# Optimization experiments

Measured on AMD Instinct MI355X. Metric: run time of the kernel, lower is better.

The kernel has to match this reference:

```python
import jax, jax.numpy as jnp
import numpy as np

B, C, H, W = 2, 256, 32, 32
D_MODEL = C
D_INNER = 2 * D_MODEL          # 512
D_STATE = 16
DT_RANK = (D_MODEL + 15) // 16  # 16
D_CONV = 4
LN_EPS = 1e-5


def setup_inputs() -> dict:
    key = jax.random.key(0)
    ks = jax.random.split(key, 32)

    def nrm(k, shape, s=0.02):
        return (jax.random.normal(k, shape) * s).astype(jnp.float32)

    inp = {"x": jax.random.normal(ks[0], (B, C, H, W), dtype=jnp.float32)}
    # LayerNorm params
    inp["ln1_w"] = jnp.ones((D_MODEL,), jnp.float32)
    inp["ln1_b"] = jnp.zeros((D_MODEL,), jnp.float32)
    inp["ln2_w"] = jnp.ones((D_MODEL,), jnp.float32)
    inp["ln2_b"] = jnp.zeros((D_MODEL,), jnp.float32)
    # Two MambaBlocks with identical structure
    for i, p in enumerate(["m1", "m2"]):
        o = 1 + i * 11
        inp[p + "_in_w"] = nrm(ks[o + 0], (D_MODEL, 2 * D_INNER))
        inp[p + "_in_b"] = jnp.zeros((2 * D_INNER,), jnp.float32)
        inp[p + "_conv_w"] = nrm(ks[o + 1], (D_INNER, 1, D_CONV), 0.1)
        inp[p + "_conv_b"] = jnp.zeros((D_INNER,), jnp.float32)
        inp[p + "_xproj_w"] = nrm(ks[o + 2], (D_INNER, DT_RANK + 2 * D_STATE))
        inp[p + "_dt_w"] = nrm(ks[o + 3], (DT_RANK, D_INNER), 0.1)
        inp[p + "_dt_b"] = (jax.random.uniform(ks[o + 4], (D_INNER,)) * 0.1 - 4.0).astype(jnp.float32)
        # S4D-real init: A[d, n] = n+1
        inp[p + "_A_log"] = jnp.log(jnp.broadcast_to(jnp.arange(1, D_STATE + 1, dtype=jnp.float32), (D_INNER, D_STATE)))
        inp[p + "_D"] = jnp.ones((D_INNER,), jnp.float32)
        inp[p + "_out_w"] = nrm(ks[o + 5], (D_INNER, D_MODEL))
        inp[p + "_out_b"] = jnp.zeros((D_MODEL,), jnp.float32)
    return inp


def layernorm(x, w, b):
    mu = jnp.mean(x, axis=-1, keepdims=True)
    var = jnp.mean(jnp.square(x - mu), axis=-1, keepdims=True)
    return (x - mu) * jax.lax.rsqrt(var + LN_EPS) * w + b


def mamba_block(x, in_w, in_b, conv_w, conv_b, xproj_w, dt_w, dt_b, A_log, Dp, out_w, out_b):
    # x: (b, h, w, c) -> flatten spatial dims into the scan sequence
    b, h, w, c = x.shape
    L = h * w
    u = x.reshape(b, L, c)
    xr = u @ in_w + in_b                       # (b, L, 2*d_inner)
    xs, res = jnp.split(xr, 2, axis=-1)
    # depthwise causal conv1d over L
    xc = jnp.transpose(xs, (0, 2, 1))          # (b, d_inner, L)
    xc = jax.lax.conv_general_dilated(
        xc, conv_w, (1,), [(D_CONV - 1, 0)],
        dimension_numbers=("NCH", "OIH", "NCH"),
        feature_group_count=D_INNER) + conv_b[None, :, None]
    xs = jax.nn.silu(jnp.transpose(xc, (0, 2, 1)))  # (b, L, d_inner)
    # input-dependent SSM params
    x_dbl = xs @ xproj_w                       # (b, L, dt_rank + 2*n)
    dt, Bm, Cm = jnp.split(x_dbl, [DT_RANK, DT_RANK + D_STATE], axis=-1)
    delta = jax.nn.softplus(dt @ dt_w + dt_b)  # (b, L, d_inner)
    A = -jnp.exp(A_log)                        # (d_inner, n)
    dA = jnp.exp(delta[..., None] * A)                         # (b, L, d, n)
    dBu = delta[..., None] * Bm[:, :, None, :] * xs[..., None]  # (b, L, d, n)

    def step(hst, ins):
        dA_t, dBu_t, C_t = ins
        hst = dA_t * hst + dBu_t               # (b, d, n)
        y_t = jnp.einsum("bdn,bn->bd", hst, C_t)
        return hst, y_t

    h0 = jnp.zeros((b, D_INNER, D_STATE), dtype=xs.dtype)
    _, ys = jax.lax.scan(step, h0,
                         (jnp.swapaxes(dA, 0, 1), jnp.swapaxes(dBu, 0, 1), jnp.swapaxes(Cm, 0, 1)))
    y = jnp.swapaxes(ys, 0, 1) + xs * Dp       # (b, L, d_inner)
    y = y * jax.nn.silu(res)
    out = y @ out_w + out_b                    # (b, L, c)
    return out.reshape(b, h, w, c)


def reference(x, ln1_w, ln1_b, ln2_w, ln2_b,
              m1_in_w, m1_in_b, m1_conv_w, m1_conv_b, m1_xproj_w, m1_dt_w, m1_dt_b, m1_A_log, m1_D, m1_out_w, m1_out_b,
              m2_in_w, m2_in_b, m2_conv_w, m2_conv_b, m2_xproj_w, m2_dt_w, m2_dt_b, m2_A_log, m2_D, m2_out_w, m2_out_b):
    xt = jnp.transpose(x, (0, 2, 3, 1))  # b c h w -> b h w c
    xt = xt + layernorm(mamba_block(xt, m1_in_w, m1_in_b, m1_conv_w, m1_conv_b, m1_xproj_w,
                                    m1_dt_w, m1_dt_b, m1_A_log, m1_D, m1_out_w, m1_out_b), ln1_w, ln1_b)
    xt = jnp.flip(xt, axis=3)  # flip channel axis, as in the original
    xt = xt + layernorm(mamba_block(xt, m2_in_w, m2_in_b, m2_conv_w, m2_conv_b, m2_xproj_w,
                                    m2_dt_w, m2_dt_b, m2_A_log, m2_D, m2_out_w, m2_out_b), ln2_w, ln2_b)
    xt = jnp.flip(xt, axis=3)
    return jnp.transpose(xt, (0, 3, 1, 2))  # b h w c -> b c h w
```

## Files before the change

kernel.cpp:

```cpp
#include <hip/hip_runtime.h>
#include <hip/hip_bf16.h>
#include <math.h>

#define L 1024
#define NB 2
#define DM 256
#define DI 512
#define DS 16
#define DR 16
#define NC 64
#define CL 16

typedef unsigned int u32;
typedef short s16x8 __attribute__((ext_vector_type(8)));
typedef float f32x4 __attribute__((ext_vector_type(4)));

__device__ __forceinline__ float sigmoidf_(float x){ return 1.f/(1.f+__expf(-x)); }

__device__ __forceinline__ unsigned short f2bf(float v){
  u32 x = __float_as_uint(v);
  u32 r = (x + 0x7fffu + ((x >> 16) & 1u)) >> 16;
  return (unsigned short)r;
}

__device__ __forceinline__ void gload_lds16(const void* g, void* l){
  __builtin_amdgcn_global_load_lds((const __attribute__((address_space(1))) u32*)g,
                                   (__attribute__((address_space(3))) u32*)l, 16, 0, 0);
}

__device__ __forceinline__ void wave_reduce2(float& a, float& b){
  #pragma unroll
  for (int m=32; m; m>>=1){ a += __shfl_xor(a, m, 64); b += __shfl_xor(b, m, 64); }
}

#define SEG1 262144
#define SEG2 294912
#define SEG3 131072
#define SEGP (SEG1+SEG2+SEG3)
__global__ __launch_bounds__(256) void k_prep(
    const float* __restrict__ inw1, const float* __restrict__ xpw1, const float* __restrict__ dtw1, const float* __restrict__ outw1,
    const float* __restrict__ inw2, const float* __restrict__ xpw2, const float* __restrict__ dtw2, const float* __restrict__ outw2,
    unsigned short* __restrict__ Wt1i, unsigned short* __restrict__ Wt1x, unsigned short* __restrict__ Wt1o,
    unsigned short* __restrict__ Wt2i, unsigned short* __restrict__ Wt2x, unsigned short* __restrict__ Wt2o){
  int g = blockIdx.x*256 + threadIdx.x;
  int p = g >= SEGP;
  int r = g - p*SEGP;
  const float* inw = p ? inw2 : inw1;  const float* xpw = p ? xpw2 : xpw1;
  const float* dtw = p ? dtw2 : dtw1;  const float* outw = p ? outw2 : outw1;
  unsigned short* Wti = p ? Wt2i : Wt1i; unsigned short* Wtx = p ? Wt2x : Wt1x;
  unsigned short* Wto = p ? Wt2o : Wt1o;
  if (r < SEG1){
    int n = r >> 8, k = r & 255;
    Wti[r] = f2bf(inw[(size_t)k*1024 + n]);
  } else if (r < SEG1+SEG2){
    int q = r - SEG1; int n = q >> 9, k = q & 511;
    float v;
    if (n < 512){
      float acc = 0.f;
      #pragma unroll
      for (int j=0;j<16;++j) acc = fmaf(xpw[k*48 + j], dtw[j*512 + n], acc);
      v = acc;
    } else if (n < 544){
      v = xpw[k*48 + 16 + (n - 512)];
    } else v = 0.f;
    Wtx[q] = f2bf(v);
  } else {
    int q = r - SEG1 - SEG2; int n = q >> 9, k = q & 511;
    Wto[q] = f2bf(outw[(size_t)k*256 + n]);
  }
}

__global__ __launch_bounds__(256) void k_transpose_in(const float* __restrict__ x,
    float* __restrict__ u, unsigned short* __restrict__ ub){
  __shared__ float T[64][65];
  int t = threadIdx.x;
  int bidx = blockIdx.x;
  int lt = bidx & 15, ct = (bidx >> 4) & 3, b = bidx >> 6;
  int l0 = lt*64, c0 = ct*64;
  int lsub = (t & 15)*4, csub = t >> 4;
  #pragma unroll
  for (int i=0;i<4;++i){
    int c = csub + i*16;
    float4 v = *(const float4*)(x + ((size_t)(b*256 + c0 + c))*1024 + l0 + lsub);
    T[lsub+0][c]=v.x; T[lsub+1][c]=v.y; T[lsub+2][c]=v.z; T[lsub+3][c]=v.w;
  }
  __syncthreads();
  int cw = (t & 15)*4, lw = t >> 4;
  #pragma unroll
  for (int i=0;i<4;++i){
    int l = lw + i*16;
    float4 v = make_float4(T[l][cw], T[l][cw+1], T[l][cw+2], T[l][cw+3]);
    size_t o = ((size_t)(b*1024 + l0 + l))*256 + c0 + cw;
    *(float4*)(u + o) = v;
    *(ushort4*)(ub + o) = make_ushort4(f2bf(v.x), f2bf(v.y), f2bf(v.z), f2bf(v.w));
  }
}

__global__ __launch_bounds__(256) void k_gemm_mfma(const unsigned short* __restrict__ A,
    const unsigned short* __restrict__ Wt, const float* __restrict__ bias,
    float* __restrict__ C, int M, int N, int K){
  __shared__ __align__(16) unsigned short As[64*64];
  __shared__ __align__(16) unsigned short Bs[64*64];
  int tid = threadIdx.x;
  int lane = tid & 63;
  int wid  = tid >> 6;
  int bm = blockIdx.y * 64, bn = blockIdx.x * 64;
  int wm = (wid >> 1) * 32, wn = (wid & 1) * 32;
  int lrow = lane & 15, lg = lane >> 4;
  int srow = tid >> 3;
  int ssl  = tid & 7;
  int sswz = ssl ^ (srow & 7);

  f32x4 acc[2][2] = {};

  for (int k0 = 0; k0 < K; k0 += 64){
    #pragma unroll
    for (int i = 0; i < 2; ++i){
      int row = srow + i*32;
      gload_lds16(A  + (size_t)(bm + row)*K + k0 + sswz*8, &As[row*64 + ssl*8]);
      gload_lds16(Wt + (size_t)(bn + row)*K + k0 + sswz*8, &Bs[row*64 + ssl*8]);
    }
    __syncthreads();
    #pragma unroll
    for (int ks = 0; ks < 2; ++ks){
      int kg = ks*4 + lg;
      int swz = (kg ^ (lrow & 7)) << 3;
      s16x8 a[2], b[2];
      #pragma unroll
      for (int f = 0; f < 2; ++f){
        a[f] = *(const s16x8*)&As[(wm + f*16 + lrow)*64 + swz];
        b[f] = *(const s16x8*)&Bs[(wn + f*16 + lrow)*64 + swz];
      }
      #pragma unroll
      for (int i = 0; i < 2; ++i)
        #pragma unroll
        for (int j = 0; j < 2; ++j)
          acc[i][j] = __builtin_amdgcn_mfma_f32_16x16x32_bf16(a[i], b[j], acc[i][j], 0, 0, 0);
    }
    __syncthreads();
  }
  #pragma unroll
  for (int j = 0; j < 2; ++j){
    int col = bn + wn + j*16 + lrow;
    if (col < N){
      float bv = bias ? bias[col] : 0.f;
      #pragma unroll
      for (int i = 0; i < 2; ++i){
        #pragma unroll
        for (int r = 0; r < 4; ++r){
          int row = bm + wm + i*16 + lg*4 + r;
          C[(size_t)row*N + col] = acc[i][j][r] + bv;
        }
      }
    }
  }
}

__global__ __launch_bounds__(256) void k_gemm_xproj(const unsigned short* __restrict__ A,
    const unsigned short* __restrict__ Wt, const float* __restrict__ dtb,
    float* __restrict__ dlt, float* __restrict__ BC, int M){
  const int K = 512;
  __shared__ __align__(16) unsigned short As[64*64];
  __shared__ __align__(16) unsigned short Bs[64*64];
  int tid = threadIdx.x;
  int lane = tid & 63;
  int wid  = tid >> 6;
  int bm = blockIdx.y * 64, bn = blockIdx.x * 64;
  int wm = (wid >> 1) * 32, wn = (wid & 1) * 32;
  int lrow = lane & 15, lg = lane >> 4;
  int srow = tid >> 3;
  int ssl  = tid & 7;
  int sswz = ssl ^ (srow & 7);

  f32x4 acc[2][2] = {};

  for (int k0 = 0; k0 < K; k0 += 64){
    #pragma unroll
    for (int i = 0; i < 2; ++i){
      int row = srow + i*32;
      gload_lds16(A  + (size_t)(bm + row)*K + k0 + sswz*8, &As[row*64 + ssl*8]);
      gload_lds16(Wt + (size_t)(bn + row)*K + k0 + sswz*8, &Bs[row*64 + ssl*8]);
    }
    __syncthreads();
    #pragma unroll
    for (int ks = 0; ks < 2; ++ks){
      int kg = ks*4 + lg;
      int swz = (kg ^ (lrow & 7)) << 3;
      s16x8 a[2], b[2];
      #pragma unroll
      for (int f = 0; f < 2; ++f){
        a[f] = *(const s16x8*)&As[(wm + f*16 + lrow)*64 + swz];
        b[f] = *(const s16x8*)&Bs[(wn + f*16 + lrow)*64 + swz];
      }
      #pragma unroll
      for (int i = 0; i < 2; ++i)
        #pragma unroll
        for (int j = 0; j < 2; ++j)
          acc[i][j] = __builtin_amdgcn_mfma_f32_16x16x32_bf16(a[i], b[j], acc[i][j], 0, 0, 0);
    }
    __syncthreads();
  }
  #pragma unroll
  for (int j = 0; j < 2; ++j){
    int col = bn + wn + j*16 + lrow;
    if (col < 512){
      float bv = dtb[col];
      #pragma unroll
      for (int i = 0; i < 2; ++i){
        #pragma unroll
        for (int r = 0; r < 4; ++r){
          int row = bm + wm + i*16 + lg*4 + r;
          float a = acc[i][j][r] + bv;
          dlt[(size_t)row*512 + col] = fmaxf(a, 0.f) + log1pf(__expf(-fabsf(a)));
        }
      }
    } else if (col < 544){
      #pragma unroll
      for (int i = 0; i < 2; ++i){
        #pragma unroll
        for (int r = 0; r < 4; ++r){
          int row = bm + wm + i*16 + lg*4 + r;
          BC[(size_t)row*32 + (col - 512)] = acc[i][j][r];
        }
      }
    }
  }
}

__global__ __launch_bounds__(256) void k_conv_silu(const float* __restrict__ xr, const float* __restrict__ cw,
    const float* __restrict__ cb, float* __restrict__ xsc, unsigned short* __restrict__ xscb){
  int g = blockIdx.x*256 + threadIdx.x;
  int d = g & 511; int l = (g >> 9) & 1023; int b = g >> 19;
  float acc = cb[d];
  const float* w = cw + d*4;
  #pragma unroll
  for (int k=0;k<4;++k){
    int j = l + k - 3;
    if (j >= 0) acc = fmaf(w[k], xr[((size_t)(b*L + j))*(2*DI) + d], acc);
  }
  float v = acc * sigmoidf_(acc);
  xsc[g] = v; xscb[g] = f2bf(v);
}

__global__ __launch_bounds__(256) void k_scan_partial(const float* __restrict__ delta, const float* __restrict__ xsc,
    const float* __restrict__ BC, const float* __restrict__ A_log,
    float* __restrict__ hend, float* __restrict__ Ssum){
  int g = blockIdx.x*256 + threadIdx.x;
  int d = g & 511; int bc = g >> 9;
  int c = bc & (NC-1); int b = bc >> 6;
  float A[DS];
  #pragma unroll
  for (int n=0;n<DS;++n) A[n] = -__expf(A_log[d*DS + n]);
  float h[DS];
  #pragma unroll
  for (int n=0;n<DS;++n) h[n] = 0.f;
  float S = 0.f;
  int l0 = c*CL;
  for (int t=0;t<CL;++t){
    size_t ix = (size_t)(b*L + l0 + t);
    float dlt = delta[ix*DI + d];
    float xv  = xsc[ix*DI + d];
    S += dlt;
    float dx = dlt * xv;
    const float* bp = BC + ix*32;
    #pragma unroll
    for (int n=0;n<DS;++n){
      float dA = __expf(dlt * A[n]);
      h[n] = fmaf(dA, h[n], dx * bp[n]);
    }
  }
  #pragma unroll
  for (int n=0;n<DS;++n) hend[((size_t)bc*DS + n)*DI + d] = h[n];
  Ssum[(size_t)bc*DI + d] = S;
}

__global__ __launch_bounds__(256) void k_scan_combine(const float* __restrict__ hend, const float* __restrict__ Ssum,
    const float* __restrict__ A_log, float* __restrict__ hinit){
  int g = blockIdx.x*256 + threadIdx.x;
  int d = g & 511; int n = (g >> 9) & 15; int b = g >> 13;
  float A = -__expf(A_log[d*DS + n]);
  float h = 0.f;
  for (int c=0;c<NC;++c){
    int bc = b*NC + c;
    hinit[((size_t)bc*DS + n)*DI + d] = h;
    float dec = __expf(A * Ssum[(size_t)bc*DI + d]);
    h = fmaf(dec, h, hend[((size_t)bc*DS + n)*DI + d]);
  }
}

__global__ __launch_bounds__(256) void k_scan_final(const float* __restrict__ delta, const float* __restrict__ xsc,
    const float* __restrict__ BC, const float* __restrict__ xr, const float* __restrict__ A_log,
    const float* __restrict__ Dp, const float* __restrict__ hinit, unsigned short* __restrict__ ygb){
  int g = blockIdx.x*256 + threadIdx.x;
  int d = g & 511; int bc = g >> 9;
  int c = bc & (NC-1); int b = bc >> 6;
  float A[DS];
  #pragma unroll
  for (int n=0;n<DS;++n) A[n] = -__expf(A_log[d*DS + n]);
  float h[DS];
  #pragma unroll
  for (int n=0;n<DS;++n) h[n] = hinit[((size_t)bc*DS + n)*DI + d];
  float Dv = Dp[d];
  int l0 = c*CL;
  for (int t=0;t<CL;++t){
    size_t ix = (size_t)(b*L + l0 + t);
    float dlt = delta[ix*DI + d];
    float xv  = xsc[ix*DI + d];
    float res = xr[ix*(2*DI) + DI + d];
    float dx = dlt * xv;
    const float* bp = BC + ix*32;
    const float* cp = bp + 16;
    float y = 0.f;
    #pragma unroll
    for (int n=0;n<DS;++n){
      float dA = __expf(dlt * A[n]);
      h[n] = fmaf(dA, h[n], dx * bp[n]);
      y = fmaf(h[n], cp[n], y);
    }
    y = fmaf(xv, Dv, y);
    ygb[ix*DI + d] = f2bf(y * (res * sigmoidf_(res)));
  }
}

__global__ __launch_bounds__(256) void k_ln_flip(const float* __restrict__ mo, const float* __restrict__ resid,
    const float* __restrict__ w, const float* __restrict__ bias,
    float* __restrict__ u2, unsigned short* __restrict__ u2b){
  int row = blockIdx.x*4 + (threadIdx.x >> 6);
  int lane = threadIdx.x & 63;
  int c4 = lane*4;
  float4 xv = *(const float4*)(mo + (size_t)row*256 + c4);
  float s1 = xv.x+xv.y+xv.z+xv.w;
  float s2 = xv.x*xv.x+xv.y*xv.y+xv.z*xv.z+xv.w*xv.w;
  wave_reduce2(s1, s2);
  float mu = s1*(1.f/256), var = s2*(1.f/256) - mu*mu;
  float inv = rsqrtf(var + 1e-5f);
  float4 rv = *(const float4*)(resid + (size_t)row*256 + c4);
  float4 wv = *(const float4*)(w + c4);
  float4 bv = *(const float4*)(bias + c4);
  float o0 = rv.x + (xv.x-mu)*inv*wv.x + bv.x;
  float o1 = rv.y + (xv.y-mu)*inv*wv.y + bv.y;
  float o2 = rv.z + (xv.z-mu)*inv*wv.z + bv.z;
  float o3 = rv.w + (xv.w-mu)*inv*wv.w + bv.w;
  size_t o = (size_t)row*256 + (252 - c4);
  *(float4*)(u2 + o) = make_float4(o3, o2, o1, o0);
  *(ushort4*)(u2b + o) = make_ushort4(f2bf(o3), f2bf(o2), f2bf(o1), f2bf(o0));
}

__global__ __launch_bounds__(256) void k_ln_out(const float* __restrict__ mo, const float* __restrict__ resid,
    const float* __restrict__ w, const float* __restrict__ bias, float* __restrict__ out){
  int row = blockIdx.x*4 + (threadIdx.x >> 6);
  int lane = threadIdx.x & 63;
  int c4 = lane*4;
  int b = row >> 10, l = row & 1023;
  float4 xv = *(const float4*)(mo + (size_t)row*256 + c4);
  float s1 = xv.x+xv.y+xv.z+xv.w;
  float s2 = xv.x*xv.x+xv.y*xv.y+xv.z*xv.z+xv.w*xv.w;
  wave_reduce2(s1, s2);
  float mu = s1*(1.f/256), var = s2*(1.f/256) - mu*mu;
  float inv = rsqrtf(var + 1e-5f);
  float4 rv = *(const float4*)(resid + (size_t)row*256 + c4);
  float4 wv = *(const float4*)(w + c4);
  float4 bv = *(const float4*)(bias + c4);
  float o0 = rv.x + (xv.x-mu)*inv*wv.x + bv.x;
  float o1 = rv.y + (xv.y-mu)*inv*wv.y + bv.y;
  float o2 = rv.z + (xv.z-mu)*inv*wv.z + bv.z;
  float o3 = rv.w + (xv.w-mu)*inv*wv.w + bv.w;
  size_t base = ((size_t)b*256 + 255) << 10;
  out[base - ((size_t)(c4+0) << 10) + l] = o0;
  out[base - ((size_t)(c4+1) << 10) + l] = o1;
  out[base - ((size_t)(c4+2) << 10) + l] = o2;
  out[base - ((size_t)(c4+3) << 10) + l] = o3;
}

static void run_block(const unsigned short* ub, const float* inb, const float* cw, const float* cb,
                      const float* dtb, const float* Alog, const float* Dp, const float* ob,
                      const unsigned short* Wti, const unsigned short* Wtx, const unsigned short* Wto,
                      float* xr, float* xsc, unsigned short* xscb, float* dlt, float* BC,
                      unsigned short* ygb, float* hend, float* hinit, float* Ssum, float* mo,
                      hipStream_t stream){
  dim3 b256(256);
  k_gemm_mfma<<<dim3(16,32), b256, 0, stream>>>(ub, Wti, inb, xr, NB*L, 2*DI, DM);
  k_conv_silu<<<4096, b256, 0, stream>>>(xr, cw, cb, xsc, xscb);
  k_gemm_xproj<<<dim3(9,32), b256, 0, stream>>>(xscb, Wtx, dtb, dlt, BC, NB*L);
  k_scan_partial<<<NB*NC*DI/256, b256, 0, stream>>>(dlt, xsc, BC, Alog, hend, Ssum);
  k_scan_combine<<<NB*DS*DI/256, b256, 0, stream>>>(hend, Ssum, Alog, hinit);
  k_scan_final<<<NB*NC*DI/256, b256, 0, stream>>>(dlt, xsc, BC, xr, Alog, Dp, hinit, ygb);
  k_gemm_mfma<<<dim3(4,32), b256, 0, stream>>>(ygb, Wto, ob, mo, NB*L, DM, DI);
}

extern "C" void kernel_launch(void* const* d_in, const int* in_sizes, int n_in,
                              void* d_out, int out_size, void* d_ws, size_t ws_size,
                              hipStream_t stream) {
  const float* x    = (const float*)d_in[0];
  const float* ln1w = (const float*)d_in[1];
  const float* ln1b = (const float*)d_in[2];
  const float* ln2w = (const float*)d_in[3];
  const float* ln2b = (const float*)d_in[4];

  const float* m1[11]; const float* m2[11];
  for (int i=0;i<11;++i){ m1[i] = (const float*)d_in[5+i]; m2[i] = (const float*)d_in[16+i]; }

  float* ws = (float*)d_ws;
  float*          u0   = ws;
  unsigned short* u0b  = (unsigned short*)(ws + 524288);
  float*          xr   = ws + 655360;
  float*          xsc  = ws + 2752512;
  unsigned short* xscb = (unsigned short*)(ws + 3801088);
  float*          dlt  = ws + 4063232;
  float*          BC   = ws + 5111808;
  unsigned short* ygb  = (unsigned short*)(ws + 5177344);
  float*          hend = ws + 5439488;
  float*          hinit= ws + 6488064;
  float*          Ssum = ws + 7536640;
  float*          u2   = ws + 7602176;
  unsigned short* Wt1i = (unsigned short*)(ws + 8126464);
  unsigned short* Wt1x = (unsigned short*)(ws + 8257536);
  unsigned short* Wt1o = (unsigned short*)(ws + 8404992);
  unsigned short* Wt2i = (unsigned short*)(ws + 8470528);
  unsigned short* Wt2x = (unsigned short*)(ws + 8601600);
  unsigned short* Wt2o = (unsigned short*)(ws + 8749056);
  unsigned short* u2b = u0b;
  float* mo = hend;

  dim3 b256(256);
  k_prep<<<2*SEGP/256, b256, 0, stream>>>(m1[0], m1[4], m1[5], m1[9],
                                          m2[0], m2[4], m2[5], m2[9],
                                          Wt1i, Wt1x, Wt1o, Wt2i, Wt2x, Wt2o);
  k_transpose_in<<<128, b256, 0, stream>>>(x, u0, u0b);

  run_block(u0b, m1[1], m1[2], m1[3], m1[6], m1[7], m1[8], m1[10],
            Wt1i, Wt1x, Wt1o, xr, xsc, xscb, dlt, BC, ygb, hend, hinit, Ssum, mo, stream);
  k_ln_flip<<<512, b256, 0, stream>>>(mo, u0, ln1w, ln1b, u2, u2b);

  run_block(u2b, m2[1], m2[2], m2[3], m2[6], m2[7], m2[8], m2[10],
            Wt2i, Wt2x, Wt2o, xr, xsc, xscb, dlt, BC, ygb, hend, hinit, Ssum, mo, stream);
  k_ln_out<<<512, b256, 0, stream>>>(mo, u2, ln2w, ln2b, (float*)d_out);
}
```

Baseline: 155.6 us.

## Fuse scan passes into one kernel, transpose intermediates to bf16 channel-major layout

```diff
diff --git a/kernel.cpp b/kernel.cpp
--- a/kernel.cpp
+++ b/kernel.cpp
@@ -7,21 +7,20 @@
 #define DM 256
 #define DI 512
 #define DS 16
-#define DR 16
 #define NC 64
 #define CL 16
 
 typedef unsigned int u32;
+typedef unsigned short u16;
 typedef short s16x8 __attribute__((ext_vector_type(8)));
 typedef float f32x4 __attribute__((ext_vector_type(4)));
 
 __device__ __forceinline__ float sigmoidf_(float x){ return 1.f/(1.f+__expf(-x)); }
-
-__device__ __forceinline__ unsigned short f2bf(float v){
+__device__ __forceinline__ u16 f2bf(float v){
   u32 x = __float_as_uint(v);
-  u32 r = (x + 0x7fffu + ((x >> 16) & 1u)) >> 16;
-  return (unsigned short)r;
-}
+  return (u16)((x + 0x7fffu + ((x >> 16) & 1u)) >> 16);
+}
+__device__ __forceinline__ float bf2f(u16 v){ return __uint_as_float((u32)v << 16); }
 
 __device__ __forceinline__ void gload_lds16(const void* g, void* l){
   __builtin_amdgcn_global_load_lds((const __attribute__((address_space(1))) u32*)g,
@@ -37,18 +36,44 @@
 #define SEG2 294912
 #define SEG3 131072
 #define SEGP (SEG1+SEG2+SEG3)
-__global__ __launch_bounds__(256) void k_prep(
+__global__ __launch_bounds__(256) void k_prep_trans(const float* __restrict__ x,
+    float* __restrict__ u, u16* __restrict__ ub,
     const float* __restrict__ inw1, const float* __restrict__ xpw1, const float* __restrict__ dtw1, const float* __restrict__ outw1,
     const float* __restrict__ inw2, const float* __restrict__ xpw2, const float* __restrict__ dtw2, const float* __restrict__ outw2,
-    unsigned short* __restrict__ Wt1i, unsigned short* __restrict__ Wt1x, unsigned short* __restrict__ Wt1o,
-    unsigned short* __restrict__ Wt2i, unsigned short* __restrict__ Wt2x, unsigned short* __restrict__ Wt2o){
-  int g = blockIdx.x*256 + threadIdx.x;
+    u16* __restrict__ Wt1i, u16* __restrict__ Wt1x, u16* __restrict__ Wt1o,
+    u16* __restrict__ Wt2i, u16* __restrict__ Wt2x, u16* __restrict__ Wt2o){
+  __shared__ float T[64][65];
+  if (blockIdx.x < 128){
+    int t = threadIdx.x;
+    int bidx = blockIdx.x;
+    int lt = bidx & 15, ct = (bidx >> 4) & 3, b = bidx >> 6;
+    int l0 = lt*64, c0 = ct*64;
+    int lsub = (t & 15)*4, csub = t >> 4;
+    #pragma unroll
+    for (int i=0;i<4;++i){
+      int c = csub + i*16;
+      float4 v = *(const float4*)(x + ((size_t)(b*256 + c0 + c))*1024 + l0 + lsub);
+      T[lsub+0][c]=v.x; T[lsub+1][c]=v.y; T[lsub+2][c]=v.z; T[lsub+3][c]=v.w;
+    }
+    __syncthreads();
+    int cw = (t & 15)*4, lw = t >> 4;
+    #pragma unroll
+    for (int i=0;i<4;++i){
+      int l = lw + i*16;
+      float4 v = make_float4(T[l][cw], T[l][cw+1], T[l][cw+2], T[l][cw+3]);
+      size_t o = ((size_t)(b*1024 + l0 + l))*256 + c0 + cw;
+      *(float4*)(u + o) = v;
+      *(ushort4*)(ub + o) = make_ushort4(f2bf(v.x), f2bf(v.y), f2bf(v.z), f2bf(v.w));
+    }
+    return;
+  }
+  int g = (blockIdx.x - 128)*256 + threadIdx.x;
   int p = g >= SEGP;
   int r = g - p*SEGP;
   const float* inw = p ? inw2 : inw1;  const float* xpw = p ? xpw2 : xpw1;
   const float* dtw = p ? dtw2 : dtw1;  const float* outw = p ? outw2 : outw1;
-  unsigned short* Wti = p ? Wt2i : Wt1i; unsigned short* Wtx = p ? Wt2x : Wt1x;
-  unsigned short* Wto = p ? Wt2o : Wt1o;
+  u16* Wti = p ? Wt2i : Wt1i; u16* Wtx = p ? Wt2x : Wt1x;
+  u16* Wto = p ? Wt2o : Wt1o;
   if (r < SEG1){
     int n = r >> 8, k = r & 255;
     Wti[r] = f2bf(inw[(size_t)k*1024 + n]);
@@ -70,49 +95,18 @@
   }
 }
 
-__global__ __launch_bounds__(256) void k_transpose_in(const float* __restrict__ x,
-    float* __restrict__ u, unsigned short* __restrict__ ub){
-  __shared__ float T[64][65];
-  int t = threadIdx.x;
-  int bidx = blockIdx.x;
-  int lt = bidx & 15, ct = (bidx >> 4) & 3, b = bidx >> 6;
-  int l0 = lt*64, c0 = ct*64;
-  int lsub = (t & 15)*4, csub = t >> 4;
-  #pragma unroll
-  for (int i=0;i<4;++i){
-    int c = csub + i*16;
-    float4 v = *(const float4*)(x + ((size_t)(b*256 + c0 + c))*1024 + l0 + lsub);
-    T[lsub+0][c]=v.x; T[lsub+1][c]=v.y; T[lsub+2][c]=v.z; T[lsub+3][c]=v.w;
-  }
-  __syncthreads();
-  int cw = (t & 15)*4, lw = t >> 4;
-  #pragma unroll
-  for (int i=0;i<4;++i){
-    int l = lw + i*16;
-    float4 v = make_float4(T[l][cw], T[l][cw+1], T[l][cw+2], T[l][cw+3]);
-    size_t o = ((size_t)(b*1024 + l0 + l))*256 + c0 + cw;
-    *(float4*)(u + o) = v;
-    *(ushort4*)(ub + o) = make_ushort4(f2bf(v.x), f2bf(v.y), f2bf(v.z), f2bf(v.w));
-  }
-}
-
-__global__ __launch_bounds__(256) void k_gemm_mfma(const unsigned short* __restrict__ A,
-    const unsigned short* __restrict__ Wt, const float* __restrict__ bias,
+__global__ __launch_bounds__(256) void k_gemm_mfma(const u16* __restrict__ A,
+    const u16* __restrict__ Wt, const float* __restrict__ bias,
     float* __restrict__ C, int M, int N, int K){
-  __shared__ __align__(16) unsigned short As[64*64];
-  __shared__ __align__(16) unsigned short Bs[64*64];
-  int tid = threadIdx.x;
-  int lane = tid & 63;
-  int wid  = tid >> 6;
+  __shared__ __align__(16) u16 As[64*64];
+  __shared__ __align__(16) u16 Bs[64*64];
+  int tid = threadIdx.x, lane = tid & 63, wid = tid >> 6;
   int bm = blockIdx.y * 64, bn = blockIdx.x * 64;
   int wm = (wid >> 1) * 32, wn = (wid & 1) * 32;
   int lrow = lane & 15, lg = lane >> 4;
-  int srow = tid >> 3;
-  int ssl  = tid & 7;
+  int srow = tid >> 3, ssl = tid & 7;
   int sswz = ssl ^ (srow & 7);
-
   f32x4 acc[2][2] = {};
-
   for (int k0 = 0; k0 < K; k0 += 64){
     #pragma unroll
     for (int i = 0; i < 2; ++i){
@@ -145,41 +139,113 @@
     if (col < N){
       float bv = bias ? bias[col] : 0.f;
       #pragma unroll
-      for (int i = 0; i < 2; ++i){
+      for (int i = 0; i < 2; ++i)
         #pragma unroll
         for (int r = 0; r < 4; ++r){
           int row = bm + wm + i*16 + lg*4 + r;
           C[(size_t)row*N + col] = acc[i][j][r] + bv;
         }
-      }
-    }
-  }
-}
-
-__global__ __launch_bounds__(256) void k_gemm_xproj(const unsigned short* __restrict__ A,
-    const unsigned short* __restrict__ Wt, const float* __restrict__ dtb,
-    float* __restrict__ dlt, float* __restrict__ BC, int M){
-  const int K = 512;
-  __shared__ __align__(16) unsigned short As[64*64];
-  __shared__ __align__(16) unsigned short Bs[64*64];
+    }
+  }
+}
+
+__global__ __launch_bounds__(256) void k_conv_t(const float* __restrict__ xr,
+    const float* __restrict__ cw, const float* __restrict__ cb,
+    u16* __restrict__ xscT, u16* __restrict__ xscbl, u16* __restrict__ sresT){
+  __shared__ float T[67*68];
   int tid = threadIdx.x;
-  int lane = tid & 63;
-  int wid  = tid >> 6;
-  int bm = blockIdx.y * 64, bn = blockIdx.x * 64;
+  int d0 = (blockIdx.x & 7) * 64;
+  int bm = (blockIdx.x >> 3) * 64;
+  bool bstart = (bm & 1023) == 0;
+  for (int base = tid; base < 67*16; base += 256){
+    int r = base >> 4, q = base & 15;
+    float4 v;
+    if (r < 3 && bstart) v = make_float4(0.f,0.f,0.f,0.f);
+    else v = *(const float4*)(xr + (size_t)(bm - 3 + r)*1024 + d0 + q*4);
+    *(float4*)&T[r*68 + q*4] = v;
+  }
+  __syncthreads();
+  int d_local = tid >> 2, lseg = tid & 3;
+  int d = d0 + d_local;
+  float4 wv = *(const float4*)(cw + d*4);
+  float cbv = cb[d];
+  float fo[16];
+  float xm3 = T[(lseg*16+0)*68 + d_local];
+  float xm2 = T[(lseg*16+1)*68 + d_local];
+  float xm1 = T[(lseg*16+2)*68 + d_local];
+  #pragma unroll
+  for (int i=0;i<16;++i){
+    float xc = T[(lseg*16+i+3)*68 + d_local];
+    float o = cbv;
+    o = fmaf(wv.x, xm3, o); o = fmaf(wv.y, xm2, o);
+    o = fmaf(wv.z, xm1, o); o = fmaf(wv.w, xc, o);
+    o *= sigmoidf_(o);
+    fo[i] = o;
+    xm3 = xm2; xm2 = xm1; xm1 = xc;
+  }
+  {
+    s16x8 v0, v1;
+    #pragma unroll
+    for (int i=0;i<8;++i){ v0[i] = (short)f2bf(fo[i]); v1[i] = (short)f2bf(fo[8+i]); }
+    u16* dst = xscT + (size_t)d*2048 + bm + lseg*16;
+    *(s16x8*)dst = v0; *(s16x8*)(dst+8) = v1;
+  }
+  __syncthreads();
+  #pragma unroll
+  for (int i=0;i<16;++i) T[(lseg*16+i+3)*68 + d_local] = fo[i];
+  __syncthreads();
+  {
+    int l_local = tid >> 2, dseg = tid & 3;
+    s16x8 p0, p1;
+    #pragma unroll
+    for (int i=0;i<8;++i){
+      p0[i] = (short)f2bf(T[(l_local+3)*68 + dseg*16 + i]);
+      p1[i] = (short)f2bf(T[(l_local+3)*68 + dseg*16 + 8 + i]);
+    }
+    u16* dst2 = xscbl + (size_t)(bm + l_local)*512 + d0 + dseg*16;
+    *(s16x8*)dst2 = p0; *(s16x8*)(dst2+8) = p1;
+  }
+  __syncthreads();
+  for (int base = tid; base < 64*16; base += 256){
+    int r = base >> 4, q = base & 15;
+    float4 v = *(const float4*)(xr + (size_t)(bm + r)*1024 + 512 + d0 + q*4);
+    v.x *= sigmoidf_(v.x); v.y *= sigmoidf_(v.y);
+    v.z *= sigmoidf_(v.z); v.w *= sigmoidf_(v.w);
+    *(float4*)&T[r*68 + q*4] = v;
+  }
+  __syncthreads();
+  {
+    s16x8 r0, r1;
+    #pragma unroll
+    for (int i=0;i<8;++i){
+      r0[i] = (short)f2bf(T[(lseg*16+i)*68 + d_local]);
+      r1[i] = (short)f2bf(T[(lseg*16+8+i)*68 + d_local]);
+    }
+    u16* dst3 = sresT + (size_t)d*2048 + bm + lseg*16;
+    *(s16x8*)dst3 = r0; *(s16x8*)(dst3+8) = r1;
+  }
+}
+
+__global__ __launch_bounds__(256) void k_xproj(const u16* __restrict__ A,
+    const u16* __restrict__ Wt, const float* __restrict__ dtb,
+    u16* __restrict__ dltT, u16* __restrict__ BCb){
+  __shared__ __align__(16) float smem[64*69];
+  u16* As = (u16*)smem;
+  u16* Bs = As + 4096;
+  int tid = threadIdx.x, lane = tid & 63, wid = tid >> 6;
+  int bn = blockIdx.x, bm = blockIdx.y * 64;
+  int bn64 = bn * 64;
   int wm = (wid >> 1) * 32, wn = (wid & 1) * 32;
   int lrow = lane & 15, lg = lane >> 4;
-  int srow = tid >> 3;
-  int ssl  = tid & 7;
+  int srow = tid >> 3, ssl = tid & 7;
   int sswz = ssl ^ (srow & 7);
-
   f32x4 acc[2][2] = {};
-
-  for (int k0 = 0; k0 < K; k0 += 64){
+  for (int k0 = 0; k0 < 512; k0 += 64){
     #pragma unroll
     for (int i = 0; i < 2; ++i){
       int row = srow + i*32;
-      gload_lds16(A  + (size_t)(bm + row)*K + k0 + sswz*8, &As[row*64 + ssl*8]);
-      gload_lds16(Wt + (size_t)(bn + row)*K + k0 + sswz*8, &Bs[row*64 + ssl*8]);
+      gload_lds16(A  + (size_t)(bm + row)*512 + k0 + sswz*8, &As[row*64 + ssl*8]);
+      gload_lds16(Wt + (size_t)(bn64 + row)*512 + k0 + sswz*8, &Bs[row*64 + ssl*8]);
     }
     __syncthreads();
     #pragma unroll
@@ -200,131 +266,143 @@
     }
     __syncthreads();
   }
-  #pragma unroll
-  for (int j = 0; j < 2; ++j){
-    int col = bn + wn + j*16 + lrow;
-    if (col < 512){
-      float bv = dtb[col];
-      #pragma unroll
-      for (int i = 0; i < 2; ++i){
+  if (bn < 8){
+    float* DT = smem;
+    #pragma unroll
+    for (int j=0;j<2;++j){
+      int col_l = wn + j*16 + lrow;
+      float bv = dtb[bn64 + col_l];
+      #pragma unroll
+      for (int i=0;i<2;++i)
         #pragma unroll
-        for (int r = 0; r < 4; ++r){
-          int row = bm + wm + i*16 + lg*4 + r;
+        for (int r=0;r<4;++r){
+          int row_l = wm + i*16 + lg*4 + r;
           float a = acc[i][j][r] + bv;
-          dlt[(size_t)row*512 + col] = fmaxf(a, 0.f) + log1pf(__expf(-fabsf(a)));
+          DT[row_l*69 + col_l] = fmaxf(a, 0.f) + log1pf(__expf(-fabsf(a)));
         }
+    }
+    __syncthreads();
+    int c_local = tid >> 2, lseg = tid & 3;
+    int dcol = bn64 + c_local;
+    s16x8 v0, v1;
+    #pragma unroll
+    for (int i=0;i<8;++i){
+      v0[i] = (short)f2bf(DT[(lseg*16+i)*69 + c_local]);
+      v1[i] = (short)f2bf(DT[(lseg*16+8+i)*69 + c_local]);
+    }
+    u16* dst = dltT + (size_t)dcol*2048 + bm + lseg*16;
+    *(s16x8*)dst = v0; *(s16x8*)(dst+8) = v1;
+  } else {
+    #pragma unroll
+    for (int j=0;j<2;++j){
+      int col_g = bn64 + wn + j*16 + lrow;
+      if (col_g < 544){
+        #pragma unroll
+        for (int i=0;i<2;++i)
+          #pragma unroll
+          for (int r=0;r<4;++r){
+            int row = bm + wm + i*16 + lg*4 + r;
+            BCb[(size_t)row*32 + (col_g - 512)] = f2bf(acc[i][j][r]);
+          }
       }
-    } else if (col < 544){
-      #pragma unroll
-      for (int i = 0; i < 2; ++i){
-        #pragma unroll
-        for (int r = 0; r < 4; ++r){
-          int row = bm + wm + i*16 + lg*4 + r;
-          BC[(size_t)row*32 + (col - 512)] = acc[i][j][r];
-        }
-      }
-    }
-  }
-}
-
-__global__ __launch_bounds__(256) void k_conv_silu(const float* __restrict__ xr, const float* __restrict__ cw,
-    const float* __restrict__ cb, float* __restrict__ xsc, unsigned short* __restrict__ xscb){
-  int g = blockIdx.x*256 + threadIdx.x;
-  int d = g & 511; int l = (g >> 9) & 1023; int b = g >> 19;
-  float acc = cb[d];
-  const float* w = cw + d*4;
-  #pragma unroll
-  for (int k=0;k<4;++k){
-    int j = l + k - 3;
-    if (j >= 0) acc = fmaf(w[k], xr[((size_t)(b*L + j))*(2*DI) + d], acc);
-  }
-  float v = acc * sigmoidf_(acc);
-  xsc[g] = v; xscb[g] = f2bf(v);
-}
-
-__global__ __launch_bounds__(256) void k_scan_partial(const float* __restrict__ delta, const float* __restrict__ xsc,
-    const float* __restrict__ BC, const float* __restrict__ A_log,
-    float* __restrict__ hend, float* __restrict__ Ssum){
-  int g = blockIdx.x*256 + threadIdx.x;
-  int d = g & 511; int bc = g >> 9;
-  int c = bc & (NC-1); int b = bc >> 6;
+    }
+  }
+}
+
+__global__ __launch_bounds__(256) void k_scan(const u16* __restrict__ dltT,
+    const u16* __restrict__ xscT, const u16* __restrict__ BCb,
+    const u16* __restrict__ sresT, const float* __restrict__ A_log,
+    const float* __restrict__ Dp, u16* __restrict__ ygb){
+  __shared__ float hbuf[64][68];
+  __shared__ float SsumL[64][4];
+  int tid = threadIdx.x;
+  int chunk = tid >> 2, dl = tid & 3;
+  int b = blockIdx.x >> 7, d0 = (blockIdx.x & 127) << 2;
+  int d = d0 + dl;
   float A[DS];
   #pragma unroll
   for (int n=0;n<DS;++n) A[n] = -__expf(A_log[d*DS + n]);
+  size_t cbase = (size_t)d*2048 + b*1024 + chunk*16;
+  s16x8 dv0 = *(const s16x8*)(dltT + cbase);
+  s16x8 dv1 = *(const s16x8*)(dltT + cbase + 8);
+  s16x8 xv0 = *(const s16x8*)(xscT + cbase);
+  s16x8 xv1 = *(const s16x8*)(xscT + cbase + 8);
+  float dr[16], xq[16];
+  #pragma unroll
+  for (int i=0;i<8;++i){
+    dr[i] = bf2f((u16)dv0[i]); dr[8+i] = bf2f((u16)dv1[i]);
+    xq[i] = bf2f((u16)xv0[i]); xq[8+i] = bf2f((u16)xv1[i]);
+  }
   float h[DS];
   #pragma unroll
   for (int n=0;n<DS;++n) h[n] = 0.f;
   float S = 0.f;
-  int l0 = c*CL;
-  for (int t=0;t<CL;++t){
-    size_t ix = (size_t)(b*L + l0 + t);
-    float dlt = delta[ix*DI + d];
-    float xv  = xsc[ix*DI + d];
-    S += dlt;
-    float dx = dlt * xv;
-    const float* bp = BC + ix*32;
-    #pragma unroll
-    for (int n=0;n<DS;++n){
-      float dA = __expf(dlt * A[n]);
-      h[n] = fmaf(dA, h[n], dx * bp[n]);
-    }
-  }
-  #pragma unroll
-  for (int n=0;n<DS;++n) hend[((size_t)bc*DS + n)*DI + d] = h[n];
-  Ssum[(size_t)bc*DI + d] = S;
-}
-
-__global__ __launch_bounds__(256) void k_scan_combine(const float* __restrict__ hend, const float* __restrict__ Ssum,
-    const float* __restrict__ A_log, float* __restrict__ hinit){
-  int g = blockIdx.x*256 + threadIdx.x;
-  int d = g & 511; int n = (g >> 9) & 15; int b = g >> 13;
-  float A = -__expf(A_log[d*DS + n]);
-  float h = 0.f;
-  for (int c=0;c<NC;++c){
-    int bc = b*NC + c;
-    hinit[((size_t)bc*DS + n)*DI + d] = h;
-    float dec = __expf(A * Ssum[(size_t)bc*DI + d]);
-    h = fmaf(dec, h, hend[((size_t)bc*DS + n)*DI + d]);
-  }
-}
-
-__global__ __launch_bounds__(256) void k_scan_final(const float* __restrict__ delta, const float* __restrict__ xsc,
-    const float* __restrict__ BC, const float* __restrict__ xr, const float* __restrict__ A_log,
-    const float* __restrict__ Dp, const float* __restrict__ hinit, unsigned short* __restrict__ ygb){
-  int g = blockIdx.x*256 + threadIdx.x;
-  int d = g & 511; int bc = g >> 9;
-  int c = bc & (NC-1); int b = bc >> 6;
-  float A[DS];
-  #pragma unroll
-  for (int n=0;n<DS;++n) A[n] = -__expf(A_log[d*DS + n]);
-  float h[DS];
-  #pragma unroll
-  for (int n=0;n<DS;++n) h[n] = hinit[((size_t)bc*DS + n)*DI + d];
+  int rbase = b*1024 + chunk*16;
+  #pragma unroll
+  for (int t=0;t<16;++t){
+    const u16* bp = BCb + (size_t)(rbase + t)*32;
+    s16x8 b0 = *(const s16x8*)bp;
+    s16x8 b1 = *(const s16x8*)(bp + 8);
+    float dlt = dr[t]; S += dlt;
+    float dx = dlt * xq[t];
+    #pragma unroll
+    for (int n=0;n<8;++n) h[n] = fmaf(__expf(dlt*A[n]), h[n], dx*bf2f((u16)b0[n]));
+    #pragma unroll
+    for (int n=0;n<8;++n) h[8+n] = fmaf(__expf(dlt*A[8+n]), h[8+n], dx*bf2f((u16)b1[n]));
+  }
+  #pragma unroll
+  for (int n=0;n<DS;++n) hbuf[chunk][dl*16+n] = h[n];
+  SsumL[chunk][dl] = S;
+  __syncthreads();
+  if (tid < 64){
+    int dl2 = tid & 3, n2 = tid >> 2;
+    float An = -__expf(A_log[(d0+dl2)*DS + n2]);
+    float hh = 0.f;
+    for (int c=0;c<NC;++c){
+      float he  = hbuf[c][dl2*16+n2];
+      float dec = __expf(An * SsumL[c][dl2]);
+      float nh  = fmaf(dec, hh, he);
+      hbuf[c][dl2*16+n2] = hh;
+      hh = nh;
+    }
+  }
+  __syncthreads();
+  #pragma unroll
+  for (int n=0;n<DS;++n) h[n] = hbuf[chunk][dl*16+n];
+  s16x8 s0 = *(const s16x8*)(sresT + cbase);
+  s16x8 s1 = *(const s16x8*)(sresT + cbase + 8);
+  float sr[16];
+  #pragma unroll
+  for (int i=0;i<8;++i){ sr[i] = bf2f((u16)s0[i]); sr[8+i] = bf2f((u16)s1[i]); }
   float Dv = Dp[d];
-  int l0 = c*CL;
-  for (int t=0;t<CL;++t){
-    size_t ix = (size_t)(b*L + l0 + t);
-    float dlt = delta[ix*DI + d];
-    float xv  = xsc[ix*DI + d];
-    float res = xr[ix*(2*DI) + DI + d];
-    float dx = dlt * xv;
-    const float* bp = BC + ix*32;
-    const float* cp = bp + 16;
+  #pragma unroll
+  for (int t=0;t<16;++t){
+    const u16* bp = BCb + (size_t)(rbase + t)*32;
+    s16x8 b0 = *(const s16x8*)bp;
+    s16x8 b1 = *(const s16x8*)(bp + 8);
+    s16x8 c0 = *(const s16x8*)(bp + 16);
+    s16x8 c1 = *(const s16x8*)(bp + 24);
+    float dlt = dr[t];
+    float dx = dlt * xq[t];
     float y = 0.f;
     #pragma unroll
-    for (int n=0;n<DS;++n){
-      float dA = __expf(dlt * A[n]);
-      h[n] = fmaf(dA, h[n], dx * bp[n]);
-      y = fmaf(h[n], cp[n], y);
-    }
-    y = fmaf(xv, Dv, y);
-    ygb[ix*DI + d] = f2bf(y * (res * sigmoidf_(res)));
+    for (int n=0;n<8;++n){
+      h[n] = fmaf(__expf(dlt*A[n]), h[n], dx*bf2f((u16)b0[n]));
+      y = fmaf(h[n], bf2f((u16)c0[n]), y);
+    }
+    #pragma unroll
+    for (int n=0;n<8;++n){
+      h[8+n] = fmaf(__expf(dlt*A[8+n]), h[8+n], dx*bf2f((u16)b1[n]));
+      y = fmaf(h[8+n], bf2f((u16)c1[n]), y);
+    }
+    y = fmaf(xq[t], Dv, y);
+    ygb[(size_t)(rbase + t)*512 + d] = f2bf(y * sr[t]);
   }
 }
 
 __global__ __launch_bounds__(256) void k_ln_flip(const float* __restrict__ mo, const float* __restrict__ resid,
     const float* __restrict__ w, const float* __restrict__ bias,
-    float* __restrict__ u2, unsigned short* __restrict__ u2b){
+    float* __restrict__ u2, u16* __restrict__ u2b){
   int row = blockIdx.x*4 + (threadIdx.x >> 6);
   int lane = threadIdx.x & 63;
   int c4 = lane*4;
@@ -372,22 +450,6 @@
   out[base - ((size_t)(c4+3) << 10) + l] = o3;
 }
 
-static void run_block(const unsigned short* ub, const float* inb, const float* cw, const float* cb,
-                      const float* dtb, const float* Alog, const float* Dp, const float* ob,
-                      const unsigned short* Wti, const unsigned short* Wtx, const unsigned short* Wto,
-                      float* xr, float* xsc, unsigned short* xscb, float* dlt, float* BC,
-                      unsigned short* ygb, float* hend, float* hinit, float* Ssum, float* mo,
-                      hipStream_t stream){
-  dim3 b256(256);
-  k_gemm_mfma<<<dim3(16,32), b256, 0, stream>>>(ub, Wti, inb, xr, NB*L, 2*DI, DM);
-  k_conv_silu<<<4096, b256, 0, stream>>>(xr, cw, cb, xsc, xscb);
-  k_gemm_xproj<<<dim3(9,32), b256, 0, stream>>>(xscb, Wtx, dtb, dlt, BC, NB*L);
-  k_scan_partial<<<NB*NC*DI/256, b256, 0, stream>>>(dlt, xsc, BC, Alog, hend, Ssum);
-  k_scan_combine<<<NB*DS*DI/256, b256, 0, stream>>>(hend, Ssum, Alog, hinit);
-  k_scan_final<<<NB*NC*DI/256, b256, 0, stream>>>(dlt, xsc, BC, xr, Alog, Dp, hinit, ygb);
-  k_gemm_mfma<<<dim3(4,32), b256, 0, stream>>>(ygb, Wto, ob, mo, NB*L, DM, DI);
-}
-
 extern "C" void kernel_launch(void* const* d_in, const int* in_sizes, int n_in,
                               void* d_out, int out_size, void* d_ws, size_t ws_size,
                               hipStream_t stream) {
@@ -401,38 +463,41 @@
   for (int i=0;i<11;++i){ m1[i] = (const float*)d_in[5+i]; m2[i] = (const float*)d_in[16+i]; }
 
   float* ws = (float*)d_ws;
-  float*          u0   = ws;
-  unsigned short* u0b  = (unsigned short*)(ws + 524288);
-  float*          xr   = ws + 655360;
-  float*          xsc  = ws + 2752512;
-  unsigned short* xscb = (unsigned short*)(ws + 3801088);
-  float*          dlt  = ws + 4063232;
-  float*          BC   = ws + 5111808;
-  unsigned short* ygb  = (unsigned short*)(ws + 5177344);
-  float*          hend = ws + 5439488;
-  float*          hinit= ws + 6488064;
-  float*          Ssum = ws + 7536640;
-  float*          u2   = ws + 7602176;
-  unsigned short* Wt1i = (unsigned short*)(ws + 8126464);
-  unsigned short* Wt1x = (unsigned short*)(ws + 8257536);
-  unsigned short* Wt1o = (unsigned short*)(ws + 8404992);
-  unsigned short* Wt2i = (unsigned short*)(ws + 8470528);
-  unsigned short* Wt2x = (unsigned short*)(ws + 8601600);
-  unsigned short* Wt2o = (unsigned short*)(ws + 8749056);
-  unsigned short* u2b = u0b;
-  float* mo = hend;
+  float* u0    = ws;
+  u16*   u0b   = (u16*)(ws + 524288);
+  float* xr    = ws + 655360;
+  u16*   xscbl = (u16*)(ws + 2752512);
+  u16*   xscT  = (u16*)(ws + 3276800);
+  u16*   sresT = (u16*)(ws + 3801088);
+  u16*   dltT  = (u16*)(ws + 4325376);
+  u16*   BCb   = (u16*)(ws + 4849664);
+  u16*   ygb   = (u16*)(ws + 4882432);
+  float* mo    = ws + 5406720;
+  float* u2    = ws + 5931008;
+  u16*   u2b   = (u16*)(ws + 6455296);
+  u16*   Wt1i  = (u16*)(ws + 6586368);
+  u16*   Wt1x  = (u16*)(ws + 6717440);
+  u16*   Wt1o  = (u16*)(ws + 6864896);
+  u16*   Wt2i  = (u16*)(ws + 6930432);
+  u16*   Wt2x  = (u16*)(ws + 7061504);
+  u16*   Wt2o  = (u16*)(ws + 7208960);
 
   dim3 b256(256);
-  k_prep<<<2*SEGP/256, b256, 0, stream>>>(m1[0], m1[4], m1[5], m1[9],
-                                          m2[0], m2[4], m2[5], m2[9],
-                                          Wt1i, Wt1x, Wt1o, Wt2i, Wt2x, Wt2o);
-  k_transpose_in<<<128, b256, 0, stream>>>(x, u0, u0b);
-
-  run_block(u0b, m1[1], m1[2], m1[3], m1[6], m1[7], m1[8], m1[10],
-            Wt1i, Wt1x, Wt1o, xr, xsc, xscb, dlt, BC, ygb, hend, hinit, Ssum, mo, stream);
+  k_prep_trans<<<128 + 2*SEGP/256, b256, 0, stream>>>(x, u0, u0b,
+      m1[0], m1[4], m1[5], m1[9], m2[0], m2[4], m2[5], m2[9],
+      Wt1i, Wt1x, Wt1o, Wt2i, Wt2x, Wt2o);
+
+  k_gemm_mfma<<<dim3(16,32), b256, 0, stream>>>(u0b, Wt1i, m1[1], xr, NB*L, 2*DI, DM);
+  k_conv_t<<<256, b256, 0, stream>>>(xr, m1[2], m1[3], xscT, xscbl, sresT);
+  k_xproj<<<dim3(9,32), b256, 0, stream>>>(xscbl, Wt1x, m1[6], dltT, BCb);
+  k_scan<<<256, b256, 0, stream>>>(dltT, xscT, BCb, sresT, m1[7], m1[8], ygb);
+  k_gemm_mfma<<<dim3(4,32), b256, 0, stream>>>(ygb, Wt1o, m1[10], mo, NB*L, DM, DI);
   k_ln_flip<<<512, b256, 0, stream>>>(mo, u0, ln1w, ln1b, u2, u2b);
 
-  run_block(u2b, m2[1], m2[2], m2[3], m2[6], m2[7], m2[8], m2[10],
-            Wt2i, Wt2x, Wt2o, xr, xsc, xscb, dlt, BC, ygb, hend, hinit, Ssum, mo, stream);
+  k_gemm_mfma<<<dim3(16,32), b256, 0, stream>>>(u2b, Wt2i, m2[1], xr, NB*L, 2*DI, DM);
+  k_conv_t<<<256, b256, 0, stream>>>(xr, m2[2], m2[3], xscT, xscbl, sresT);
+  k_xproj<<<dim3(9,32), b256, 0, stream>>>(xscbl, Wt2x, m2[6], dltT, BCb);
+  k_scan<<<256, b256, 0, stream>>>(dltT, xscT, BCb, sresT, m2[7], m2[8], ygb);
+  k_gemm_mfma<<<dim3(4,32), b256, 0, stream>>>(ygb, Wt2o, m2[10], mo, NB*L, DM, DI);
   k_ln_out<<<512, b256, 0, stream>>>(mo, u2, ln2w, ln2b, (float*)d_out);
 }
```

After: 128.1 us. 17.7% less time.
